# Optimization experiments

Hardware: AMD Instinct MI355X
Metric: run time of the kernel (lower is better)

Reference implementation:

```python
import jax, jax.numpy as jnp
import numpy as np

B, S, HID = 4, 4096, 2048
H, G = 16, 4
D = HID // H  # head_dim = 128
KV = HID * G // H  # k/v proj out dim = 512


def setup_inputs() -> dict:
    key = jax.random.key(0)
    ks = jax.random.split(key, 9)
    s = lambda fan_in: 1.0 / np.sqrt(fan_in)
    return {
        "hidden_states": jax.random.normal(ks[0], (B, S, HID), jnp.float32),
        "Wq": jax.random.uniform(ks[1], (HID, HID), jnp.float32, -s(HID), s(HID)),
        "bq": jnp.zeros((HID,), jnp.float32),
        "Wk": jax.random.uniform(ks[2], (HID, KV), jnp.float32, -s(HID), s(HID)),
        "bk": jnp.zeros((KV,), jnp.float32),
        "Wv": jax.random.uniform(ks[3], (HID, KV), jnp.float32, -s(HID), s(HID)),
        "bv": jnp.zeros((KV,), jnp.float32),
        "Wo": jax.random.uniform(ks[4], (HID, HID), jnp.float32, -s(HID), s(HID)),
        "bo": jnp.zeros((HID,), jnp.float32),
    }


def reference(hidden_states, Wq, bq, Wk, bk, Wv, bv, Wo, bo):
    # Projections (torch Linear: x @ W^T + b; here W stored as [in, out])
    q = hidden_states @ Wq + bq            # [B,S,HID]
    k = hidden_states @ Wk + bk            # [B,S,KV]
    v = hidden_states @ Wv + bv            # [B,S,KV]
    q = q.reshape(B, S, H, D)
    k = k.reshape(B, S, G, D)
    v = v.reshape(B, S, G, D)
    # Faithful to source: scores over groups at the SAME position, [B,S,H,G]
    scores = jnp.einsum("bshd,bsgd->bshg", q, k) / jnp.sqrt(jnp.float32(D))
    probs = jax.nn.softmax(scores, axis=-1)  # softmax over G
    out = jnp.einsum("bshg,bsgd->bshd", probs, v)  # [B,S,H,D]
    out = out.reshape(B, S, HID)
    return out @ Wo + bo
```

## Files before the change

kernel.cpp:

```cpp
#include <hip/hip_runtime.h>
#include <hip/hip_bf16.h>
#include <stdint.h>

typedef __bf16 bf16_t;
typedef __bf16 bf16x8 __attribute__((ext_vector_type(8)));
typedef __bf16 bf16x4_t __attribute__((ext_vector_type(4)));
typedef float f32x4 __attribute__((ext_vector_type(4)));

#define AS1 __attribute__((address_space(1)))
#define AS3 __attribute__((address_space(3)))

__device__ __forceinline__ void stage16(const bf16_t* g, char* l) {
    __builtin_amdgcn_global_load_lds((const AS1 uint32_t*)g, (AS3 uint32_t*)l, 16, 0, 0);
}

#define BAR()   __builtin_amdgcn_s_barrier()
#define LGKM0() asm volatile("s_waitcnt lgkmcnt(0)" ::: "memory")
#define VMC(N)  asm volatile("s_waitcnt vmcnt(" #N ")" ::: "memory")
#define PRIO(p) __builtin_amdgcn_s_setprio(p)

template <typename OutT>
__global__ __launch_bounds__(512, 2) void gemm256(
    const bf16_t* __restrict__ A, int lda,
    const bf16_t* __restrict__ Bt, int ldb,
    const float* __restrict__ bias,
    OutT* __restrict__ C, int ldc,
    int K, int nTilesN)
{
    __shared__ char smem[131072];
    const int tid  = threadIdx.x;
    const int wave = tid >> 6;
    const int lane = tid & 63;
    const int wm = wave >> 2;
    const int wn = wave & 3;

    const int bid = blockIdx.x;
    const int swz = (bid & 7) * ((int)gridDim.x >> 3) + (bid >> 3);
    const int m0 = (swz / nTilesN) << 8;
    const int n0 = (swz % nTilesN) << 8;

    const int srow = lane >> 2;
    const int scol = ((lane & 3) * 8) ^ ((lane & 32) >> 1);
    const bf16_t* aS0 = A  + (size_t)(m0 + wave * 32 + srow) * lda + scol;
    const bf16_t* aS1 = aS0 + (size_t)16 * lda;
    const bf16_t* bS0 = Bt + (size_t)(n0 + wave * 32 + srow) * ldb + scol;
    const bf16_t* bS1 = bS0 + (size_t)16 * ldb;

#define STAGE_A(b,kk,kb) do { \
    stage16(aS0 + (kb) + (kk)*32, smem + (b)*65536 + (kk)*16384 + wave*2048); \
    stage16(aS1 + (kb) + (kk)*32, smem + (b)*65536 + (kk)*16384 + wave*2048 + 1024); } while(0)
#define STAGE_B(b,kk,kb) do { \
    stage16(bS0 + (kb) + (kk)*32, smem + (b)*65536 + 32768 + (kk)*16384 + wave*2048); \
    stage16(bS1 + (kb) + (kk)*32, smem + (b)*65536 + 32768 + (kk)*16384 + wave*2048 + 1024); } while(0)

    const int rdLane = (lane & 15) * 64 + (((lane >> 4) * 16) ^ ((lane & 8) << 2));
    const char* aRdB = smem + rdLane + wm * 8192;
    const char* bRdB = smem + 32768 + rdLane + wn * 4096;

    f32x4 acc[8][4];
#pragma unroll
    for (int i = 0; i < 8; ++i)
#pragma unroll
        for (int j = 0; j < 4; ++j) acc[i][j] = (f32x4){0.f, 0.f, 0.f, 0.f};
    bf16x8 a[8], bf0, bf1;

#define READ_A(b,kk) { _Pragma("unroll") \
    for (int mi = 0; mi < 8; ++mi) \
        a[mi] = *(const bf16x8*)(aRdB + (b)*65536 + (kk)*16384 + mi*1024); }
#define READ_B(b,kk,nh) { \
    bf0 = *(const bf16x8*)(bRdB + (b)*65536 + (kk)*16384 + (nh)*2048); \
    bf1 = *(const bf16x8*)(bRdB + (b)*65536 + (kk)*16384 + (nh)*2048 + 1024); }
#define MFMA_H(nh) { _Pragma("unroll") \
    for (int mi = 0; mi < 8; ++mi) { \
        acc[mi][(nh)*2]   = __builtin_amdgcn_mfma_f32_16x16x32_bf16(a[mi], bf0, acc[mi][(nh)*2],   0, 0, 0); \
        acc[mi][(nh)*2+1] = __builtin_amdgcn_mfma_f32_16x16x32_bf16(a[mi], bf1, acc[mi][(nh)*2+1], 0, 0, 0); } }
#define PHASE(RDS, STG, MF, WAIT) do { \
    RDS; STG; BAR(); LGKM0(); PRIO(1); MF; PRIO(0); WAIT; BAR(); } while(0)

    STAGE_A(0, 0, 0);  STAGE_B(0, 0, 0);  STAGE_A(0, 1, 0);  STAGE_B(0, 1, 0);
    STAGE_A(1, 0, 64); STAGE_B(1, 0, 64); STAGE_A(1, 1, 64);
    VMC(6);
    BAR();

    const int NI = K >> 7;
    for (int it = 0; it < NI - 1; ++it) {
        const int kB  = (it << 7) + 64;
        const int kN0 = (it << 7) + 128;
        const int kN1 = (it << 7) + 192;
        PHASE(READ_A(0,0); READ_B(0,0,0), STAGE_B(1,1,kB),  MFMA_H(0), );
        PHASE(READ_B(0,0,1),              STAGE_A(0,0,kN0), MFMA_H(1), );
        PHASE(READ_A(0,1); READ_B(0,1,0), STAGE_B(0,0,kN0), MFMA_H(0), );
        PHASE(READ_B(0,1,1),              STAGE_A(0,1,kN0), MFMA_H(1), VMC(6));
        PHASE(READ_A(1,0); READ_B(1,0,0), STAGE_B(0,1,kN0), MFMA_H(0), );
        PHASE(READ_B(1,0,1),              STAGE_A(1,0,kN1), MFMA_H(1), );
        PHASE(READ_A(1,1); READ_B(1,1,0), STAGE_B(1,0,kN1), MFMA_H(0), );
        PHASE(READ_B(1,1,1),              STAGE_A(1,1,kN1), MFMA_H(1), VMC(6));
    }
    {
        const int kB = ((NI - 1) << 7) + 64;
        PHASE(READ_A(0,0); READ_B(0,0,0), STAGE_B(1,1,kB), MFMA_H(0), );
        PHASE(READ_B(0,0,1),             ,                 MFMA_H(1), );
        PHASE(READ_A(0,1); READ_B(0,1,0),,                 MFMA_H(0), );
        PHASE(READ_B(0,1,1),             ,                 MFMA_H(1), VMC(0));
        PHASE(READ_A(1,0); READ_B(1,0,0),,                 MFMA_H(0), );
        PHASE(READ_B(1,0,1),             ,                 MFMA_H(1), );
        PHASE(READ_A(1,1); READ_B(1,1,0),,                 MFMA_H(0), );
        READ_B(1,1,1); BAR(); LGKM0(); PRIO(1); MFMA_H(1); PRIO(0);
    }

    const int mrow = lane & 15;
    const int quad = lane >> 4;
    const int cb = n0 + wn * 64 + mrow;
    const int rb = m0 + wm * 128 + quad * 4;
#pragma unroll
    for (int ni = 0; ni < 4; ++ni) {
        const int col = cb + ni * 16;
        const float bv = bias[col];
#pragma unroll
        for (int mi = 0; mi < 8; ++mi) {
            const int row = rb + mi * 16;
#pragma unroll
            for (int r = 0; r < 4; ++r)
                C[(size_t)(row + r) * ldc + col] = (OutT)(acc[mi][ni][r] + bv);
        }
    }
#undef STAGE_A
#undef STAGE_B
#undef READ_A
#undef READ_B
#undef MFMA_H
#undef PHASE
}

__global__ __launch_bounds__(256) void f32_to_bf16(const float* __restrict__ src,
                                                   bf16_t* __restrict__ dst, int n4) {
    int i = blockIdx.x * 256 + threadIdx.x;
    if (i >= n4) return;
    float4 v = ((const float4*)src)[i];
    bf16x4_t o;
    o.x = (bf16_t)v.x; o.y = (bf16_t)v.y; o.z = (bf16_t)v.z; o.w = (bf16_t)v.w;
    ((bf16x4_t*)dst)[i] = o;
}

__global__ __launch_bounds__(256) void transpose_convert(
    const float* __restrict__ src, bf16_t* __restrict__ dst,
    int rows, int cols)
{
    __shared__ bf16_t t[64][65];
    const int tx = threadIdx.x & 63;
    const int ty = threadIdx.x >> 6;
    const int c0 = blockIdx.x * 64;
    const int r0 = blockIdx.y * 64;
#pragma unroll
    for (int r = ty; r < 64; r += 4)
        t[r][tx] = (bf16_t)src[(size_t)(r0 + r) * cols + c0 + tx];
    __syncthreads();
#pragma unroll
    for (int r = ty; r < 64; r += 4)
        dst[(size_t)(c0 + r) * rows + r0 + tx] = t[tx][r];
}

__global__ void concat_bias(const float* __restrict__ bq, const float* __restrict__ bk,
                            const float* __restrict__ bv, float* __restrict__ o) {
    int i = blockIdx.x * 256 + threadIdx.x;
    if (i >= 3072) return;
    o[i] = (i < 2048) ? bq[i] : (i < 2560 ? bk[i - 2048] : bv[i - 2560]);
}

__global__ __launch_bounds__(256) void gqa_attn(
    const bf16_t* __restrict__ q, int sq,
    const bf16_t* __restrict__ kv, int skv,
    bf16_t* __restrict__ out, int so)
{
    const int token = blockIdx.x;
    const int wave = threadIdx.x >> 6, lane = threadIdx.x & 63;
    const bf16_t* qb  = q  + (size_t)token * sq;
    const bf16_t* kvb = kv + (size_t)token * skv;
    const float scale = 0.08838834764831845f;
    float k0[4], k1[4], v0[4], v1[4];
#pragma unroll
    for (int g = 0; g < 4; ++g) {
        uint32_t ku = *(const uint32_t*)(kvb + g * 128 + lane * 2);
        k0[g] = __uint_as_float(ku << 16);
        k1[g] = __uint_as_float(ku & 0xffff0000u);
        uint32_t vu = *(const uint32_t*)(kvb + 512 + g * 128 + lane * 2);
        v0[g] = __uint_as_float(vu << 16);
        v1[g] = __uint_as_float(vu & 0xffff0000u);
    }
#pragma unroll
    for (int hh = 0; hh < 4; ++hh) {
        const int h = wave * 4 + hh;
        uint32_t qu = *(const uint32_t*)(qb + h * 128 + lane * 2);
        float q0 = __uint_as_float(qu << 16);
        float q1 = __uint_as_float(qu & 0xffff0000u);
        float s[4];
#pragma unroll
        for (int g = 0; g < 4; ++g) s[g] = q0 * k0[g] + q1 * k1[g];
#pragma unroll
        for (int off = 32; off > 0; off >>= 1)
#pragma unroll
            for (int g = 0; g < 4; ++g) s[g] += __shfl_xor(s[g], off);
        float mx = fmaxf(fmaxf(s[0], s[1]), fmaxf(s[2], s[3]));
        float e[4], sum = 0.f;
#pragma unroll
        for (int g = 0; g < 4; ++g) { e[g] = __expf((s[g] - mx) * scale); sum += e[g]; }
        const float rs = 1.0f / sum;
        float o0 = 0.f, o1 = 0.f;
#pragma unroll
        for (int g = 0; g < 4; ++g) { o0 += e[g] * v0[g]; o1 += e[g] * v1[g]; }
        o0 *= rs; o1 *= rs;
        bf16_t* op = out + (size_t)token * so + h * 128 + lane * 2;
        op[0] = (bf16_t)o0;
        op[1] = (bf16_t)o1;
    }
}

extern "C" void kernel_launch(void* const* d_in, const int* in_sizes, int n_in,
                              void* d_out, int out_size, void* d_ws, size_t ws_size,
                              hipStream_t stream) {
    const float* hs = (const float*)d_in[0];
    const float* Wq = (const float*)d_in[1];
    const float* bq = (const float*)d_in[2];
    const float* Wk = (const float*)d_in[3];
    const float* bk = (const float*)d_in[4];
    const float* Wv = (const float*)d_in[5];
    const float* bv = (const float*)d_in[6];
    const float* Wo = (const float*)d_in[7];
    const float* bo = (const float*)d_in[8];
    float* outp = (float*)d_out;
    char* ws = (char*)d_ws;

    bf16_t* Wt     = (bf16_t*)(ws);
    bf16_t* Wot    = (bf16_t*)(ws + 12582912);
    float*  bqkv   = (float*)(ws + 20971520);
    bf16_t* hs_b   = (bf16_t*)(ws + 20983808);
    bf16_t* atto   = (bf16_t*)(ws + 20983808);
    bf16_t* qkv    = (bf16_t*)d_out;

    f32_to_bf16<<<32768, 256, 0, stream>>>(hs, hs_b, 8388608);
    transpose_convert<<<dim3(32, 32), 256, 0, stream>>>(Wq, Wt, 2048, 2048);
    transpose_convert<<<dim3(8, 32), 256, 0, stream>>>(Wk, Wt + (size_t)2048 * 2048, 2048, 512);
    transpose_convert<<<dim3(8, 32), 256, 0, stream>>>(Wv, Wt + (size_t)2560 * 2048, 2048, 512);
    transpose_convert<<<dim3(32, 32), 256, 0, stream>>>(Wo, Wot, 2048, 2048);
    concat_bias<<<12, 256, 0, stream>>>(bq, bk, bv, bqkv);

    gemm256<bf16_t><<<768, 512, 0, stream>>>(hs_b, 2048, Wt, 2048, bqkv, qkv, 3072, 2048, 12);
    gqa_attn<<<16384, 256, 0, stream>>>(qkv, 3072, qkv + 2048, 3072, atto, 2048);
    gemm256<float><<<512, 512, 0, stream>>>(atto, 2048, Wot, 2048, bo, outp, 2048, 2048, 8);
}
```

Before: 679.9 us.

## Restructure GEMM inner loop to hold B fragments and stage epilogue via LDS

The inner loop now loads all B fragments for a buffer once and keeps them in registers, then streams A in pairs of M tiles across four phases per buffer. The staging order is changed to match. The epilogue now writes biased results into shared memory with an XOR swizzle and copies them out as coalesced 16-byte row stores, one half-tile at a time. This targets the scattered scalar global stores and redundant B reads, at the cost of extra barriers and shared-memory round trips in the epilogue.

```diff
diff --git a/kernel.cpp b/kernel.cpp
--- a/kernel.cpp
+++ b/kernel.cpp
@@ -62,24 +62,28 @@
     for (int i = 0; i < 8; ++i)
 #pragma unroll
         for (int j = 0; j < 4; ++j) acc[i][j] = (f32x4){0.f, 0.f, 0.f, 0.f};
-    bf16x8 a[8], bf0, bf1;
-
-#define READ_A(b,kk) { _Pragma("unroll") \
-    for (int mi = 0; mi < 8; ++mi) \
-        a[mi] = *(const bf16x8*)(aRdB + (b)*65536 + (kk)*16384 + mi*1024); }
-#define READ_B(b,kk,nh) { \
-    bf0 = *(const bf16x8*)(bRdB + (b)*65536 + (kk)*16384 + (nh)*2048); \
-    bf1 = *(const bf16x8*)(bRdB + (b)*65536 + (kk)*16384 + (nh)*2048 + 1024); }
-#define MFMA_H(nh) { _Pragma("unroll") \
-    for (int mi = 0; mi < 8; ++mi) { \
-        acc[mi][(nh)*2]   = __builtin_amdgcn_mfma_f32_16x16x32_bf16(a[mi], bf0, acc[mi][(nh)*2],   0, 0, 0); \
-        acc[mi][(nh)*2+1] = __builtin_amdgcn_mfma_f32_16x16x32_bf16(a[mi], bf1, acc[mi][(nh)*2+1], 0, 0, 0); } }
-#define PHASE(RDS, STG, MF, WAIT) do { \
-    RDS; STG; BAR(); LGKM0(); PRIO(1); MF; PRIO(0); WAIT; BAR(); } while(0)
-
-    STAGE_A(0, 0, 0);  STAGE_B(0, 0, 0);  STAGE_A(0, 1, 0);  STAGE_B(0, 1, 0);
-    STAGE_A(1, 0, 64); STAGE_B(1, 0, 64); STAGE_A(1, 1, 64);
-    VMC(6);
+    bf16x8 bfr[2][4];
+    bf16x8 af[2][2];
+
+#define RDB8(b) { _Pragma("unroll") \
+    for (int kk = 0; kk < 2; ++kk) _Pragma("unroll") \
+        for (int ni = 0; ni < 4; ++ni) \
+            bfr[kk][ni] = *(const bf16x8*)(bRdB + (b)*65536 + kk*16384 + ni*1024); }
+#define RDA(b,mp) { _Pragma("unroll") \
+    for (int t = 0; t < 2; ++t) _Pragma("unroll") \
+        for (int kk = 0; kk < 2; ++kk) \
+            af[t][kk] = *(const bf16x8*)(aRdB + (b)*65536 + kk*16384 + ((mp)*2+t)*1024); }
+#define MF(mp) { _Pragma("unroll") \
+    for (int t = 0; t < 2; ++t) _Pragma("unroll") \
+        for (int ni = 0; ni < 4; ++ni) _Pragma("unroll") \
+            for (int kk = 0; kk < 2; ++kk) \
+                acc[(mp)*2+t][ni] = __builtin_amdgcn_mfma_f32_16x16x32_bf16(af[t][kk], bfr[kk][ni], acc[(mp)*2+t][ni], 0, 0, 0); }
+#define PHASE(RDS, STG, MFM, WAIT) do { \
+    RDS; STG; BAR(); LGKM0(); PRIO(1); MFM; PRIO(0); WAIT; BAR(); } while(0)
+
+    STAGE_A(0, 0, 0);  STAGE_A(0, 1, 0);  STAGE_B(0, 0, 0);  STAGE_B(0, 1, 0);
+    STAGE_B(1, 0, 64); STAGE_B(1, 1, 64);
+    VMC(4);
     BAR();
 
     const int NI = K >> 7;
@@ -87,48 +91,71 @@
         const int kB  = (it << 7) + 64;
         const int kN0 = (it << 7) + 128;
         const int kN1 = (it << 7) + 192;
-        PHASE(READ_A(0,0); READ_B(0,0,0), STAGE_B(1,1,kB),  MFMA_H(0), );
-        PHASE(READ_B(0,0,1),              STAGE_A(0,0,kN0), MFMA_H(1), );
-        PHASE(READ_A(0,1); READ_B(0,1,0), STAGE_B(0,0,kN0), MFMA_H(0), );
-        PHASE(READ_B(0,1,1),              STAGE_A(0,1,kN0), MFMA_H(1), VMC(6));
-        PHASE(READ_A(1,0); READ_B(1,0,0), STAGE_B(0,1,kN0), MFMA_H(0), );
-        PHASE(READ_B(1,0,1),              STAGE_A(1,0,kN1), MFMA_H(1), );
-        PHASE(READ_A(1,1); READ_B(1,1,0), STAGE_B(1,0,kN1), MFMA_H(0), );
-        PHASE(READ_B(1,1,1),              STAGE_A(1,1,kN1), MFMA_H(1), VMC(6));
+        PHASE(RDB8(0); RDA(0,0), STAGE_A(1,0,kB),  MF(0), );
+        PHASE(RDA(0,1),          STAGE_A(1,1,kB),  MF(1), );
+        PHASE(RDA(0,2),          STAGE_B(0,0,kN0), MF(2), );
+        PHASE(RDA(0,3),          STAGE_B(0,1,kN0), MF(3), VMC(4));
+        PHASE(RDB8(1); RDA(1,0), STAGE_A(0,0,kN0), MF(0), );
+        PHASE(RDA(1,1),          STAGE_A(0,1,kN0), MF(1), );
+        PHASE(RDA(1,2),          STAGE_B(1,0,kN1), MF(2), );
+        PHASE(RDA(1,3),          STAGE_B(1,1,kN1), MF(3), VMC(4));
     }
     {
         const int kB = ((NI - 1) << 7) + 64;
-        PHASE(READ_A(0,0); READ_B(0,0,0), STAGE_B(1,1,kB), MFMA_H(0), );
-        PHASE(READ_B(0,0,1),             ,                 MFMA_H(1), );
-        PHASE(READ_A(0,1); READ_B(0,1,0),,                 MFMA_H(0), );
-        PHASE(READ_B(0,1,1),             ,                 MFMA_H(1), VMC(0));
-        PHASE(READ_A(1,0); READ_B(1,0,0),,                 MFMA_H(0), );
-        PHASE(READ_B(1,0,1),             ,                 MFMA_H(1), );
-        PHASE(READ_A(1,1); READ_B(1,1,0),,                 MFMA_H(0), );
-        READ_B(1,1,1); BAR(); LGKM0(); PRIO(1); MFMA_H(1); PRIO(0);
-    }
-
-    const int mrow = lane & 15;
-    const int quad = lane >> 4;
-    const int cb = n0 + wn * 64 + mrow;
-    const int rb = m0 + wm * 128 + quad * 4;
-#pragma unroll
-    for (int ni = 0; ni < 4; ++ni) {
-        const int col = cb + ni * 16;
-        const float bv = bias[col];
-#pragma unroll
-        for (int mi = 0; mi < 8; ++mi) {
-            const int row = rb + mi * 16;
-#pragma unroll
-            for (int r = 0; r < 4; ++r)
-                C[(size_t)(row + r) * ldc + col] = (OutT)(acc[mi][ni][r] + bv);
+        PHASE(RDB8(0); RDA(0,0), STAGE_A(1,0,kB), MF(0), );
+        PHASE(RDA(0,1),          STAGE_A(1,1,kB), MF(1), );
+        PHASE(RDA(0,2),          ,                MF(2), );
+        PHASE(RDA(0,3),          ,                MF(3), VMC(0));
+        PHASE(RDB8(1); RDA(1,0), ,                MF(0), );
+        PHASE(RDA(1,1),          ,                MF(1), );
+        PHASE(RDA(1,2),          ,                MF(2), );
+        RDA(1,3); BAR(); LGKM0(); PRIO(1); MF(3); PRIO(0);
+    }
+    BAR();
+
+    {
+        const int mrow = lane & 15;
+        const int quad = lane >> 4;
+        constexpr int CSZ = (int)sizeof(OutT);
+        float bias_v[4];
+#pragma unroll
+        for (int ni = 0; ni < 4; ++ni)
+            bias_v[ni] = bias[n0 + wn * 64 + ni * 16 + mrow];
+#pragma unroll
+        for (int h = 0; h < 2; ++h) {
+            if (wm == h) {
+#pragma unroll
+                for (int ni = 0; ni < 4; ++ni) {
+                    const int colb = (wn * 64 + ni * 16 + mrow) * CSZ;
+#pragma unroll
+                    for (int mi = 0; mi < 8; ++mi)
+#pragma unroll
+                        for (int r = 0; r < 4; ++r) {
+                            const int lrow = mi * 16 + quad * 4 + r;
+                            *(OutT*)(smem + lrow * 256 * CSZ + (colb ^ (quad * 16 * CSZ))) =
+                                (OutT)(acc[mi][ni][r] + bias_v[ni]);
+                        }
+                }
+            }
+            BAR();
+            const int ROUNDS = 128 * 256 * CSZ / 8192;
+#pragma unroll
+            for (int rd = 0; rd < ROUNDS; ++rd) {
+                const int flat = rd * 8192 + tid * 16;
+                const int lrow = flat / (256 * CSZ);
+                const int colb = flat % (256 * CSZ);
+                const int q2 = (lrow >> 2) & 3;
+                uint4 v = *(const uint4*)(smem + lrow * 256 * CSZ + (colb ^ (q2 * 16 * CSZ)));
+                *(uint4*)((char*)C + ((size_t)(m0 + h * 128 + lrow) * ldc + n0) * CSZ + colb) = v;
+            }
+            BAR();
         }
     }
 #undef STAGE_A
 #undef STAGE_B
-#undef READ_A
-#undef READ_B
-#undef MFMA_H
+#undef RDB8
+#undef RDA
+#undef MF
 #undef PHASE
 }
 
```

New measurement: 632.8 us. 1.07x faster.
